# Kernel tuning notes

Hardware: AMD Instinct MI355X
Metric: run time of the kernel (lower is better)

Reference implementation:

```python
import jax, jax.numpy as jnp
import numpy as np
import math

B, S, U, H = 2, 2048, 1024, 16
DK = U // H  # 64


def setup_inputs() -> dict:
    key = jax.random.key(0)
    ks = jax.random.split(key, 12)
    scale = 1.0 / math.sqrt(U)
    inp = {
        "query": jax.random.normal(ks[0], (B, S, U), dtype=jnp.float32),
        "key": jax.random.normal(ks[1], (B, S, U), dtype=jnp.float32),
        "value": jax.random.normal(ks[2], (B, S, U), dtype=jnp.float32),
        # causal mask, broadcast over batch: 1 = attend, 0 = masked
        "mask": jnp.broadcast_to(jnp.tril(jnp.ones((S, S), dtype=bool)), (B, S, S)),
        # nn.Linear params (torch convention: y = x @ W.T + b)
        "Wq": jax.random.uniform(ks[3], (U, U), jnp.float32, -scale, scale),
        "bq": jax.random.uniform(ks[4], (U,), jnp.float32, -scale, scale),
        "Wk": jax.random.uniform(ks[5], (U, U), jnp.float32, -scale, scale),
        "bk": jax.random.uniform(ks[6], (U,), jnp.float32, -scale, scale),
        "Wv": jax.random.uniform(ks[7], (U, U), jnp.float32, -scale, scale),
        "bv": jax.random.uniform(ks[8], (U,), jnp.float32, -scale, scale),
        "Wo": jax.random.uniform(ks[9], (U, U), jnp.float32, -scale, scale),
        "bo": jax.random.uniform(ks[10], (U,), jnp.float32, -scale, scale),
    }
    return inp


def reference(query, key, value, mask, Wq, bq, Wk, bk, Wv, bv, Wo, bo):
    b = query.shape[0]
    # QKV projections -> [b, H, S, DK]
    q = (query @ Wq.T + bq).reshape(b, -1, H, DK).transpose(0, 2, 1, 3)
    k = (key @ Wk.T + bk).reshape(b, -1, H, DK).transpose(0, 2, 1, 3)
    v = (value @ Wv.T + bv).reshape(b, -1, H, DK).transpose(0, 2, 1, 3)
    # scaled dot-product scores [b, H, Sq, Sk]
    scores = jnp.einsum("bhqd,bhkd->bhqk", q, k) / math.sqrt(DK)
    scores = jnp.where(mask[:, None, :, :], scores, jnp.float32(-1e9))
    A = jax.nn.softmax(scores, axis=-1)
    # dropout is eval/identity (p effectively inactive in reference)
    Hout = jnp.einsum("bhqk,bhkd->bhqd", A, v)
    H_concat = Hout.transpose(0, 2, 1, 3).reshape(b, -1, U)
    return H_concat @ Wo.T + bo
```

## Files before the change

### kernel.cpp

```cpp
#include <hip/hip_runtime.h>
#include <math.h>

#define B_NUM 2
#define S_LEN 2048
#define U_DIM 1024
#define H_NUM 16
#define DK 64
#define M_TOT (B_NUM * S_LEN)

typedef __attribute__((ext_vector_type(8))) short bf8;
typedef __attribute__((ext_vector_type(4))) float f4;

__device__ __forceinline__ unsigned short f2bf(float f) {
    union { float f; unsigned int u; } x; x.f = f;
    unsigned int r = x.u + 0x7fffu + ((x.u >> 16) & 1u);
    return (unsigned short)(r >> 16);
}

__device__ __forceinline__ void gl2lds16(const void* g, void* l) {
    __builtin_amdgcn_global_load_lds(
        (const __attribute__((address_space(1))) unsigned int*)g,
        (__attribute__((address_space(3))) unsigned int*)l, 16, 0, 0);
}

struct CvtArgs {
    const float* src[7];
    unsigned short* dst[7];
    int n[7];
};

__global__ __launch_bounds__(256) void convert_bf16(CvtArgs a)
{
    const int seg = blockIdx.y;
    const int i = (blockIdx.x * 256 + threadIdx.x) * 8;
    if (i >= a.n[seg]) return;
    const float* s = a.src[seg] + i;
    float4 v0 = *(const float4*)s;
    float4 v1 = *(const float4*)(s + 4);
    unsigned int p0 = (unsigned)f2bf(v0.x) | ((unsigned)f2bf(v0.y) << 16);
    unsigned int p1 = (unsigned)f2bf(v0.z) | ((unsigned)f2bf(v0.w) << 16);
    unsigned int p2 = (unsigned)f2bf(v1.x) | ((unsigned)f2bf(v1.y) << 16);
    unsigned int p3 = (unsigned)f2bf(v1.z) | ((unsigned)f2bf(v1.w) << 16);
    uint4 o = {p0, p1, p2, p3};
    *(uint4*)(a.dst[seg] + i) = o;
}

struct GemmLds {
    unsigned short As[2][128][32];
    unsigned short Bs[2][128][32];
};

template <int OMODE>
__device__ __forceinline__ void gemm_core(
    GemmLds& S,
    const unsigned short* __restrict__ A, const unsigned short* __restrict__ W,
    const float* __restrict__ bias, void* __restrict__ Cv, float scale,
    int bx, int by)
{
    const int tid = threadIdx.x;
    const int w = tid >> 6, lane = tid & 63;
    const int quad = lane >> 4, cid = lane & 15;
    const int wy = w >> 1, wx = w & 1;
    const int m0 = by * 128, n0 = bx * 128;

    const int row_s = tid >> 1;
    const int sp = tid & 1;
    const int rr = (row_s >> 2) & 3;
    const int p0 = (2 * sp + rr) & 3;
    const int p1 = (2 * sp + 1 + rr) & 3;

    const unsigned short* gA = A + (size_t)(m0 + row_s) * U_DIM + 16 * sp;
    const unsigned short* gB = W + (size_t)(n0 + row_s) * U_DIM + 16 * sp;

    uint4 a0, a1, b0, b1;
#define GPF(k0_) do {                                   \
        a0 = *(const uint4*)(gA + (k0_));               \
        a1 = *(const uint4*)(gA + (k0_) + 8);           \
        b0 = *(const uint4*)(gB + (k0_));               \
        b1 = *(const uint4*)(gB + (k0_) + 8);           \
    } while (0)

    f4 acc[4][4] = {};

    GPF(0);
    *(uint4*)&S.As[0][row_s][p0 * 8] = a0;
    *(uint4*)&S.As[0][row_s][p1 * 8] = a1;
    *(uint4*)&S.Bs[0][row_s][p0 * 8] = b0;
    *(uint4*)&S.Bs[0][row_s][p1 * 8] = b1;
    GPF(32);
    __syncthreads();

#pragma unroll 2
    for (int k0 = 0; k0 < U_DIM; k0 += 32) {
        const int cur = (k0 >> 5) & 1;
        if (k0 + 32 < U_DIM) {
            const int nxt = cur ^ 1;
            *(uint4*)&S.As[nxt][row_s][p0 * 8] = a0;
            *(uint4*)&S.As[nxt][row_s][p1 * 8] = a1;
            *(uint4*)&S.Bs[nxt][row_s][p0 * 8] = b0;
            *(uint4*)&S.Bs[nxt][row_s][p1 * 8] = b1;
            if (k0 + 64 < U_DIM) GPF(k0 + 64);
        }

        bf8 af[4], bfr[4];
#pragma unroll
        for (int mt = 0; mt < 4; ++mt) {
            int row = wy * 64 + mt * 16 + cid;
            int seg = (quad + (row >> 2)) & 3;
            af[mt] = *(const bf8*)&S.As[cur][row][seg * 8];
        }
#pragma unroll
        for (int nt = 0; nt < 4; ++nt) {
            int row = wx * 64 + nt * 16 + cid;
            int seg = (quad + (row >> 2)) & 3;
            bfr[nt] = *(const bf8*)&S.Bs[cur][row][seg * 8];
        }
#pragma unroll
        for (int mt = 0; mt < 4; ++mt)
#pragma unroll
            for (int nt = 0; nt < 4; ++nt)
                acc[mt][nt] = __builtin_amdgcn_mfma_f32_16x16x32_bf16(
                    af[mt], bfr[nt], acc[mt][nt], 0, 0, 0);
        __syncthreads();
    }
#undef GPF

#pragma unroll
    for (int nt = 0; nt < 4; ++nt) {
        int col = n0 + wx * 64 + nt * 16 + cid;
        float bv = bias[col];
#pragma unroll
        for (int mt = 0; mt < 4; ++mt) {
            int rowb = m0 + wy * 64 + mt * 16 + quad * 4;
#pragma unroll
            for (int i = 0; i < 4; ++i) {
                float v = (acc[mt][nt][i] + bv) * scale;
                if constexpr (OMODE == 0) {
                    ((unsigned short*)Cv)[(size_t)(rowb + i) * U_DIM + col] = f2bf(v);
                } else if constexpr (OMODE == 1) {
                    ((float*)Cv)[(size_t)(rowb + i) * U_DIM + col] = v;
                } else {
                    int bb = rowb >> 11;
                    int ss = (rowb & (S_LEN - 1)) + i;
                    size_t idx = ((size_t)(bb * H_NUM + (col >> 6)) * DK + (col & 63))
                                 * S_LEN + ss;
                    ((unsigned short*)Cv)[idx] = f2bf(v);
                }
            }
        }
    }
}

struct QkvArgs {
    const unsigned short* A[3];
    const unsigned short* W[3];
    const float* bias[3];
    unsigned short* C[3];
    float scale[3];
};

__global__ __launch_bounds__(256, 3) void gemm_qkv(QkvArgs a) {
    __shared__ GemmLds S;
    const int L = (int)blockIdx.x + 8 * ((int)blockIdx.y + 32 * (int)blockIdx.z);
    const int xcd = L & 7, j = L >> 3;
    const int z = j >> 5, r = j & 31;
    const int by = xcd * 4 + (r & 3);
    const int bx = r >> 2;
    if (z == 2)
        gemm_core<2>(S, a.A[2], a.W[2], a.bias[2], a.C[2], a.scale[2], bx, by);
    else
        gemm_core<0>(S, a.A[z], a.W[z], a.bias[z], a.C[z], a.scale[z], bx, by);
}

__global__ __launch_bounds__(256, 3) void gemm_obf(
    const unsigned short* __restrict__ A, const unsigned short* __restrict__ W,
    const float* __restrict__ bias, float* __restrict__ C) {
    __shared__ GemmLds S;
    const int L = (int)blockIdx.x + 8 * (int)blockIdx.y;
    const int xcd = L & 7, j = L >> 3;
    const int by = xcd * 4 + (j & 3);
    const int bx = j >> 2;
    gemm_core<1>(S, A, W, bias, C, 1.0f, bx, by);
}

__global__ __launch_bounds__(256, 4) void attn_mfma(
    const unsigned short* __restrict__ Q, const unsigned short* __restrict__ K,
    const unsigned short* __restrict__ VT, unsigned short* __restrict__ O)
{
    __shared__ __align__(16) unsigned short Ks[128][64];
    __shared__ __align__(16) unsigned short Vs[64][128];

    const int L = (int)blockIdx.x + 32 * ((int)blockIdx.y + 16 * (int)blockIdx.z);
    const int xcd = L & 7;
    const int j   = L >> 3;
    const int gl  = j & 3;
    const int i   = j >> 2;
    const int hb  = (xcd << 2) | gl;
    const int h = hb & 15, b = hb >> 4;
    const int px = i & 7, pk = i >> 3;
    const int qt = (pk == 0) ? 31 - px : (pk == 1) ? 16 + px
                 : (pk == 2) ? 15 - px : px;

    const int q0 = qt * 64;
    const int tid = threadIdx.x, w = tid >> 6, lane = tid & 63;
    const int quad = lane >> 4, cid = lane & 15;

#define KFRAG(r, s) (*(const bf8*)&Ks[r][(((s) ^ ((r) & 7)) * 8)])
#define VFRAG(r, s) (*(const bf8*)&Vs[r][(((((s) & 8) | (((s) ^ (r)) & 7))) * 8)])

    unsigned short (*QsA)[64] = (unsigned short (*)[64])&Ks[0][0];
    const int srow8 = lane >> 3;
    const int sw = ((lane & 7) ^ srow8) * 8;
    {
        const unsigned short* qg =
            Q + ((size_t)b * S_LEN + q0 + w * 16 + srow8) * U_DIM + h * DK + sw;
        gl2lds16(qg, &QsA[w * 16][0]);
        gl2lds16(qg + 8 * U_DIM, &QsA[w * 16 + 8][0]);
    }
    __syncthreads();
    const bf8 qfa = *(const bf8*)&QsA[w * 16 + cid][(((quad) ^ (cid & 7)) * 8)];
    const bf8 qfb = *(const bf8*)&QsA[w * 16 + cid][((((quad + 4)) ^ (cid & 7)) * 8)];

    const unsigned short* kgl =
        K + ((size_t)b * S_LEN + w * 32 + srow8) * U_DIM + h * DK + (lane & 7) * 8;
    const int vr0 = lane >> 4;
    const int s16 = lane & 15;
    const unsigned short* vgl =
        VT + ((size_t)(b * H_NUM + h) * DK + w * 16 + vr0) * S_LEN + s16 * 8;
    const int spE = (((s16 & 8) | ((s16 ^ vr0) & 7))) * 8;
    const int spO = (((s16 & 8) | ((s16 ^ (vr0 + 4)) & 7))) * 8;
    const int ksw = ((lane & 7) ^ srow8) * 8;

    uint4 kr0, kr1, kr2, kr3, vq0, vq1, vq2, vq3;
#define PREFETCH(kt_) do {                                                    \
        const unsigned short* kp_ = kgl + (size_t)(kt_) * 128 * U_DIM;        \
        kr0 = *(const uint4*)(kp_);                                           \
        kr1 = *(const uint4*)(kp_ + (size_t)8 * U_DIM);                       \
        kr2 = *(const uint4*)(kp_ + (size_t)16 * U_DIM);                      \
        kr3 = *(const uint4*)(kp_ + (size_t)24 * U_DIM);                      \
        const unsigned short* vp_ = vgl + (kt_) * 128;                        \
        vq0 = *(const uint4*)(vp_);                                           \
        vq1 = *(const uint4*)(vp_ + (size_t)4 * S_LEN);                       \
        vq2 = *(const uint4*)(vp_ + (size_t)8 * S_LEN);                       \
        vq3 = *(const uint4*)(vp_ + (size_t)12 * S_LEN);                      \
    } while (0)

    f4 o[4] = {};
    float l_p = 0.0f;
    const int qrow = q0 + w * 16 + cid;

    const int nkt = (qt >> 1) + 1;
    PREFETCH(0);

    for (int kt = 0; kt < nkt; ++kt) {
        __syncthreads();
        *(uint4*)&Ks[w * 32 + 0  + srow8][ksw] = kr0;
        *(uint4*)&Ks[w * 32 + 8  + srow8][ksw] = kr1;
        *(uint4*)&Ks[w * 32 + 16 + srow8][ksw] = kr2;
        *(uint4*)&Ks[w * 32 + 24 + srow8][ksw] = kr3;
        *(uint4*)&Vs[w * 16 + 0  + vr0][spE] = vq0;
        *(uint4*)&Vs[w * 16 + 4  + vr0][spO] = vq1;
        *(uint4*)&Vs[w * 16 + 8  + vr0][spE] = vq2;
        *(uint4*)&Vs[w * 16 + 12 + vr0][spO] = vq3;
        __syncthreads();
        if (kt + 1 < nkt) PREFETCH(kt + 1);

        f4 sc[8];
#pragma unroll
        for (int t = 0; t < 8; ++t) {
            int r = t * 16 + cid;
            f4 a = {};
            a = __builtin_amdgcn_mfma_f32_16x16x32_bf16(KFRAG(r, quad), qfa, a, 0, 0, 0);
            a = __builtin_amdgcn_mfma_f32_16x16x32_bf16(KFRAG(r, quad + 4), qfb, a, 0, 0, 0);
            sc[t] = a;
        }

        if (kt == nkt - 1) {
#pragma unroll
            for (int t = 0; t < 8; ++t) {
#pragma unroll
                for (int i2 = 0; i2 < 4; ++i2) {
                    int key = kt * 128 + t * 16 + quad * 4 + i2;
                    if (key > qrow) sc[t][i2] = -1e30f;
                }
            }
        }

#pragma unroll
        for (int t = 0; t < 8; ++t) {
#pragma unroll
            for (int i2 = 0; i2 < 4; ++i2) {
                float p = exp2f(sc[t][i2]);
                sc[t][i2] = p;
                l_p += p;
            }
        }

        unsigned int r_[8], r2_[8];
#pragma unroll
        for (int t = 0; t < 8; ++t) {
            asm("v_cvt_pk_bf16_f32 %0, %1, %2"
                : "=v"(r_[t]) : "v"(sc[t][0]), "v"(sc[t][1]));
            asm("v_cvt_pk_bf16_f32 %0, %1, %2"
                : "=v"(r2_[t]) : "v"(sc[t][2]), "v"(sc[t][3]));
        }

        const bool qodd = (quad & 1) != 0;
#pragma unroll
        for (int f = 0; f < 4; ++f) {
            unsigned int xa = r_[2 * f], ya = r_[2 * f + 1];
            asm("v_permlane32_swap_b32 %0, %1" : "+v"(xa), "+v"(ya));
            unsigned int xas = __builtin_amdgcn_ds_swizzle((int)xa, 0x401f);
            unsigned int yas = __builtin_amdgcn_ds_swizzle((int)ya, 0x401f);
            unsigned int xb = r2_[2 * f], yb = r2_[2 * f + 1];
            asm("v_permlane32_swap_b32 %0, %1" : "+v"(xb), "+v"(yb));
            unsigned int xbs = __builtin_amdgcn_ds_swizzle((int)xb, 0x401f);
            unsigned int ybs = __builtin_amdgcn_ds_swizzle((int)yb, 0x401f);
            unsigned int u0 = qodd ? yas : xa;
            unsigned int u1 = qodd ? ybs : xb;
            unsigned int u2 = qodd ? ya : xas;
            unsigned int u3 = qodd ? yb : xbs;
            union { uint4 u; bf8 v; } pf;
            pf.u = (uint4){u0, u1, u2, u3};
#pragma unroll
            for (int t = 0; t < 4; ++t) {
                int r = t * 16 + cid;
                o[t] = __builtin_amdgcn_mfma_f32_16x16x32_bf16(
                    pf.v, VFRAG(r, 4 * f + quad), o[t], 0, 0, 0);
            }
        }
    }
#undef PREFETCH
#undef KFRAG
#undef VFRAG

    float l = l_p;
    l += __shfl_xor(l, 16);
    l += __shfl_xor(l, 32);
    const float inv = 1.0f / l;
#pragma unroll
    for (int i2 = 0; i2 < 4; ++i2) {
        float invi = __shfl(inv, (lane & 48) | (quad * 4 + i2));
        int rowg = q0 + w * 16 + quad * 4 + i2;
        size_t rbase = ((size_t)b * S_LEN + rowg) * U_DIM + h * DK;
#pragma unroll
        for (int t = 0; t < 4; ++t)
            O[rbase + t * 16 + cid] = f2bf(o[t][i2] * invi);
    }
}

extern "C" void kernel_launch(void* const* d_in, const int* in_sizes, int n_in,
                              void* d_out, int out_size, void* d_ws, size_t ws_size,
                              hipStream_t stream)
{
    const float* query = (const float*)d_in[0];
    const float* key   = (const float*)d_in[1];
    const float* value = (const float*)d_in[2];
    const float* Wq = (const float*)d_in[4];
    const float* bq = (const float*)d_in[5];
    const float* Wk = (const float*)d_in[6];
    const float* bk = (const float*)d_in[7];
    const float* Wv = (const float*)d_in[8];
    const float* bv = (const float*)d_in[9];
    const float* Wo = (const float*)d_in[10];
    const float* bo = (const float*)d_in[11];
    float* out = (float*)d_out;

    const size_t ACT = (size_t)M_TOT * U_DIM;
    const size_t WT  = (size_t)U_DIM * U_DIM;

    unsigned short* xq  = (unsigned short*)d_ws;
    unsigned short* xk  = xq + ACT;
    unsigned short* xv  = xk + ACT;
    unsigned short* wqb = xv + ACT;
    unsigned short* wkb = wqb + WT;
    unsigned short* wvb = wkb + WT;
    unsigned short* wob = wvb + WT;
    unsigned short* qg  = wob + WT;
    unsigned short* kg  = qg + ACT;
    unsigned short* vg  = kg + ACT;
    unsigned short* vt  = vg + ACT;
    unsigned short* ao  = vt + ACT;

    CvtArgs ca;
    ca.src[0] = query; ca.dst[0] = xq;  ca.n[0] = (int)ACT;
    ca.src[1] = key;   ca.dst[1] = xk;  ca.n[1] = (int)ACT;
    ca.src[2] = value; ca.dst[2] = xv;  ca.n[2] = (int)ACT;
    ca.src[3] = Wq;    ca.dst[3] = wqb; ca.n[3] = (int)WT;
    ca.src[4] = Wk;    ca.dst[4] = wkb; ca.n[4] = (int)WT;
    ca.src[5] = Wv;    ca.dst[5] = wvb; ca.n[5] = (int)WT;
    ca.src[6] = Wo;    ca.dst[6] = wob; ca.n[6] = (int)WT;
    convert_bf16<<<dim3(ACT / (256 * 8), 7), 256, 0, stream>>>(ca);

    QkvArgs ga;
    ga.A[0] = xq; ga.W[0] = wqb; ga.bias[0] = bq; ga.C[0] = qg;
    ga.scale[0] = 0.125f * 1.44269504088896340736f;
    ga.A[1] = xk; ga.W[1] = wkb; ga.bias[1] = bk; ga.C[1] = kg; ga.scale[1] = 1.0f;
    ga.A[2] = xv; ga.W[2] = wvb; ga.bias[2] = bv; ga.C[2] = vt; ga.scale[2] = 1.0f;
    gemm_qkv<<<dim3(U_DIM / 128, M_TOT / 128, 3), 256, 0, stream>>>(ga);

    attn_mfma<<<dim3(S_LEN / 64, H_NUM, B_NUM), 256, 0, stream>>>(qg, kg, vt, ao);

    gemm_obf<<<dim3(U_DIM / 128, M_TOT / 128), 256, 0, stream>>>(ao, wob, bo, out);
}
```

Baseline: 224.6 us.

## Fuse fp32-to-bf16 conversion into GEMM tile loads, drop separate convert kernel

Removes the standalone conversion kernel that cast activations and weights to bf16 in workspace. The GEMMs now load fp32 tiles directly and pack them to bf16 with v_cvt_pk_bf16_f32 before the LDS store. This avoids one launch and the write-then-reread of bf16 copies. In exchange, each GEMM reads twice the global bytes per tile, repeated across tiles, and uses more registers for the prefetch.

```diff
diff --git a/kernel.cpp b/kernel.cpp
--- a/kernel.cpp
+++ b/kernel.cpp
@@ -17,43 +17,30 @@
     return (unsigned short)(r >> 16);
 }
 
+__device__ __forceinline__ unsigned int pkbf(float a, float b) {
+    unsigned int r;
+    asm("v_cvt_pk_bf16_f32 %0, %1, %2" : "=v"(r) : "v"(a), "v"(b));
+    return r;
+}
+__device__ __forceinline__ uint4 pack8(float4 u, float4 v) {
+    return (uint4){pkbf(u.x, u.y), pkbf(u.z, u.w), pkbf(v.x, v.y), pkbf(v.z, v.w)};
+}
+
 __device__ __forceinline__ void gl2lds16(const void* g, void* l) {
     __builtin_amdgcn_global_load_lds(
         (const __attribute__((address_space(1))) unsigned int*)g,
         (__attribute__((address_space(3))) unsigned int*)l, 16, 0, 0);
 }
 
-struct CvtArgs {
-    const float* src[7];
-    unsigned short* dst[7];
-    int n[7];
-};
-
-__global__ __launch_bounds__(256) void convert_bf16(CvtArgs a)
-{
-    const int seg = blockIdx.y;
-    const int i = (blockIdx.x * 256 + threadIdx.x) * 8;
-    if (i >= a.n[seg]) return;
-    const float* s = a.src[seg] + i;
-    float4 v0 = *(const float4*)s;
-    float4 v1 = *(const float4*)(s + 4);
-    unsigned int p0 = (unsigned)f2bf(v0.x) | ((unsigned)f2bf(v0.y) << 16);
-    unsigned int p1 = (unsigned)f2bf(v0.z) | ((unsigned)f2bf(v0.w) << 16);
-    unsigned int p2 = (unsigned)f2bf(v1.x) | ((unsigned)f2bf(v1.y) << 16);
-    unsigned int p3 = (unsigned)f2bf(v1.z) | ((unsigned)f2bf(v1.w) << 16);
-    uint4 o = {p0, p1, p2, p3};
-    *(uint4*)(a.dst[seg] + i) = o;
-}
-
 struct GemmLds {
     unsigned short As[2][128][32];
     unsigned short Bs[2][128][32];
 };
 
-template <int OMODE>
+template <int OMODE, bool AF32>
 __device__ __forceinline__ void gemm_core(
     GemmLds& S,
-    const unsigned short* __restrict__ A, const unsigned short* __restrict__ W,
+    const void* __restrict__ Av, const float* __restrict__ Wf,
     const float* __restrict__ bias, void* __restrict__ Cv, float scale,
     int bx, int by)
 {
@@ -69,24 +56,46 @@
     const int p0 = (2 * sp + rr) & 3;
     const int p1 = (2 * sp + 1 + rr) & 3;
 
-    const unsigned short* gA = A + (size_t)(m0 + row_s) * U_DIM + 16 * sp;
-    const unsigned short* gB = W + (size_t)(n0 + row_s) * U_DIM + 16 * sp;
-
-    uint4 a0, a1, b0, b1;
-#define GPF(k0_) do {                                   \
-        a0 = *(const uint4*)(gA + (k0_));               \
-        a1 = *(const uint4*)(gA + (k0_) + 8);           \
-        b0 = *(const uint4*)(gB + (k0_));               \
-        b1 = *(const uint4*)(gB + (k0_) + 8);           \
+    const unsigned short* gA =
+        (const unsigned short*)Av + (size_t)(m0 + row_s) * U_DIM + 16 * sp;
+    const float* gAf =
+        (const float*)Av + (size_t)(m0 + row_s) * U_DIM + 16 * sp;
+    const float* gBf = Wf + (size_t)(n0 + row_s) * U_DIM + 16 * sp;
+
+    uint4 a0, a1;
+    float4 fa0, fa1, fa2, fa3, fb0, fb1, fb2, fb3;
+#define GPF(k0_) do {                                       \
+        if constexpr (AF32) {                               \
+            fa0 = *(const float4*)(gAf + (k0_));            \
+            fa1 = *(const float4*)(gAf + (k0_) + 4);        \
+            fa2 = *(const float4*)(gAf + (k0_) + 8);        \
+            fa3 = *(const float4*)(gAf + (k0_) + 12);       \
+        } else {                                            \
+            a0 = *(const uint4*)(gA + (k0_));               \
+            a1 = *(const uint4*)(gA + (k0_) + 8);           \
+        }                                                   \
+        fb0 = *(const float4*)(gBf + (k0_));                \
+        fb1 = *(const float4*)(gBf + (k0_) + 4);            \
+        fb2 = *(const float4*)(gBf + (k0_) + 8);            \
+        fb3 = *(const float4*)(gBf + (k0_) + 12);           \
     } while (0)
 
+#define STORE(buf_) do {                                    \
+        uint4 ta0, ta1;                                     \
+        if constexpr (AF32) {                               \
+            ta0 = pack8(fa0, fa1); ta1 = pack8(fa2, fa3);   \
+        } else { ta0 = a0; ta1 = a1; }                      \
+        uint4 tb0 = pack8(fb0, fb1), tb1 = pack8(fb2, fb3); \
+        *(uint4*)&S.As[buf_][row_s][p0 * 8] = ta0;          \
+        *(uint4*)&S.As[buf_][row_s][p1 * 8] = ta1;          \
+        *(uint4*)&S.Bs[buf_][row_s][p0 * 8] = tb0;          \
+        *(uint4*)&S.Bs[buf_][row_s][p1 * 8] = tb1;          \
+    } while (0)
+
     f4 acc[4][4] = {};
 
     GPF(0);
-    *(uint4*)&S.As[0][row_s][p0 * 8] = a0;
-    *(uint4*)&S.As[0][row_s][p1 * 8] = a1;
-    *(uint4*)&S.Bs[0][row_s][p0 * 8] = b0;
-    *(uint4*)&S.Bs[0][row_s][p1 * 8] = b1;
+    STORE(0);
     GPF(32);
     __syncthreads();
 
@@ -94,11 +103,7 @@
     for (int k0 = 0; k0 < U_DIM; k0 += 32) {
         const int cur = (k0 >> 5) & 1;
         if (k0 + 32 < U_DIM) {
-            const int nxt = cur ^ 1;
-            *(uint4*)&S.As[nxt][row_s][p0 * 8] = a0;
-            *(uint4*)&S.As[nxt][row_s][p1 * 8] = a1;
-            *(uint4*)&S.Bs[nxt][row_s][p0 * 8] = b0;
-            *(uint4*)&S.Bs[nxt][row_s][p1 * 8] = b1;
+            STORE(cur ^ 1);
             if (k0 + 64 < U_DIM) GPF(k0 + 64);
         }
 
@@ -124,6 +129,7 @@
         __syncthreads();
     }
 #undef GPF
+#undef STORE
 
 #pragma unroll
     for (int nt = 0; nt < 4; ++nt) {
@@ -152,8 +158,8 @@
 }
 
 struct QkvArgs {
-    const unsigned short* A[3];
-    const unsigned short* W[3];
+    const void* A[3];
+    const float* W[3];
     const float* bias[3];
     unsigned short* C[3];
     float scale[3];
@@ -167,20 +173,20 @@
     const int by = xcd * 4 + (r & 3);
     const int bx = r >> 2;
     if (z == 2)
-        gemm_core<2>(S, a.A[2], a.W[2], a.bias[2], a.C[2], a.scale[2], bx, by);
+        gemm_core<2, true>(S, a.A[2], a.W[2], a.bias[2], a.C[2], a.scale[2], bx, by);
     else
-        gemm_core<0>(S, a.A[z], a.W[z], a.bias[z], a.C[z], a.scale[z], bx, by);
+        gemm_core<0, true>(S, a.A[z], a.W[z], a.bias[z], a.C[z], a.scale[z], bx, by);
 }
 
 __global__ __launch_bounds__(256, 3) void gemm_obf(
-    const unsigned short* __restrict__ A, const unsigned short* __restrict__ W,
+    const unsigned short* __restrict__ A, const float* __restrict__ W,
     const float* __restrict__ bias, float* __restrict__ C) {
     __shared__ GemmLds S;
     const int L = (int)blockIdx.x + 8 * (int)blockIdx.y;
     const int xcd = L & 7, j = L >> 3;
     const int by = xcd * 4 + (j & 3);
     const int bx = j >> 2;
-    gemm_core<1>(S, A, W, bias, C, 1.0f, bx, by);
+    gemm_core<1, false>(S, A, W, bias, C, 1.0f, bx, by);
 }
 
 __global__ __launch_bounds__(256, 4) void attn_mfma(
@@ -299,10 +305,8 @@
         unsigned int r_[8], r2_[8];
 #pragma unroll
         for (int t = 0; t < 8; ++t) {
-            asm("v_cvt_pk_bf16_f32 %0, %1, %2"
-                : "=v"(r_[t]) : "v"(sc[t][0]), "v"(sc[t][1]));
-            asm("v_cvt_pk_bf16_f32 %0, %1, %2"
-                : "=v"(r2_[t]) : "v"(sc[t][2]), "v"(sc[t][3]));
+            r_[t]  = pkbf(sc[t][0], sc[t][1]);
+            r2_[t] = pkbf(sc[t][2], sc[t][3]);
         }
 
         const bool qodd = (quad & 1) != 0;
@@ -367,39 +371,20 @@
     float* out = (float*)d_out;
 
     const size_t ACT = (size_t)M_TOT * U_DIM;
-    const size_t WT  = (size_t)U_DIM * U_DIM;
-
-    unsigned short* xq  = (unsigned short*)d_ws;
-    unsigned short* xk  = xq + ACT;
-    unsigned short* xv  = xk + ACT;
-    unsigned short* wqb = xv + ACT;
-    unsigned short* wkb = wqb + WT;
-    unsigned short* wvb = wkb + WT;
-    unsigned short* wob = wvb + WT;
-    unsigned short* qg  = wob + WT;
-    unsigned short* kg  = qg + ACT;
-    unsigned short* vg  = kg + ACT;
-    unsigned short* vt  = vg + ACT;
-    unsigned short* ao  = vt + ACT;
-
-    CvtArgs ca;
-    ca.src[0] = query; ca.dst[0] = xq;  ca.n[0] = (int)ACT;
-    ca.src[1] = key;   ca.dst[1] = xk;  ca.n[1] = (int)ACT;
-    ca.src[2] = value; ca.dst[2] = xv;  ca.n[2] = (int)ACT;
-    ca.src[3] = Wq;    ca.dst[3] = wqb; ca.n[3] = (int)WT;
-    ca.src[4] = Wk;    ca.dst[4] = wkb; ca.n[4] = (int)WT;
-    ca.src[5] = Wv;    ca.dst[5] = wvb; ca.n[5] = (int)WT;
-    ca.src[6] = Wo;    ca.dst[6] = wob; ca.n[6] = (int)WT;
-    convert_bf16<<<dim3(ACT / (256 * 8), 7), 256, 0, stream>>>(ca);
+
+    unsigned short* qg = (unsigned short*)d_ws;
+    unsigned short* kg = qg + ACT;
+    unsigned short* vt = kg + ACT;
+    unsigned short* ao = vt + ACT;
 
     QkvArgs ga;
-    ga.A[0] = xq; ga.W[0] = wqb; ga.bias[0] = bq; ga.C[0] = qg;
+    ga.A[0] = query; ga.W[0] = Wq; ga.bias[0] = bq; ga.C[0] = qg;
     ga.scale[0] = 0.125f * 1.44269504088896340736f;
-    ga.A[1] = xk; ga.W[1] = wkb; ga.bias[1] = bk; ga.C[1] = kg; ga.scale[1] = 1.0f;
-    ga.A[2] = xv; ga.W[2] = wvb; ga.bias[2] = bv; ga.C[2] = vt; ga.scale[2] = 1.0f;
+    ga.A[1] = key;   ga.W[1] = Wk; ga.bias[1] = bk; ga.C[1] = kg; ga.scale[1] = 1.0f;
+    ga.A[2] = value; ga.W[2] = Wv; ga.bias[2] = bv; ga.C[2] = vt; ga.scale[2] = 1.0f;
     gemm_qkv<<<dim3(U_DIM / 128, M_TOT / 128, 3), 256, 0, stream>>>(ga);
 
     attn_mfma<<<dim3(S_LEN / 64, H_NUM, B_NUM), 256, 0, stream>>>(qg, kg, vt, ao);
 
-    gemm_obf<<<dim3(U_DIM / 128, M_TOT / 128), 256, 0, stream>>>(ao, wob, bo, out);
-}
+    gemm_obf<<<dim3(U_DIM / 128, M_TOT / 128), 256, 0, stream>>>(ao, Wo, bo, out);
+}
```

Result: slower. 248.4 us (+10.6%).

## Stage GEMM tiles with direct global-to-LDS loads and use packed bf16 conversion

Applied to the files above, without the earlier changes.

The GEMM main loop now fills shared memory with global_load_lds, loading straight into LDS with a swizzled source column, instead of loading into registers and then storing to LDS. The sync moves to the top of the loop. This frees registers and removes the VGPR-to-LDS store instructions. The fp32-to-bf16 convert kernel now uses the hardware v_cvt_pk_bf16_f32 instruction in place of manual rounding, and an unused workspace buffer is dropped. The prefetch distance shrinks to one stage, so less global latency is hidden per iteration.

```diff
diff --git a/kernel.cpp b/kernel.cpp
--- a/kernel.cpp
+++ b/kernel.cpp
@@ -15,6 +15,12 @@
     union { float f; unsigned int u; } x; x.f = f;
     unsigned int r = x.u + 0x7fffu + ((x.u >> 16) & 1u);
     return (unsigned short)(r >> 16);
+}
+
+__device__ __forceinline__ unsigned int pkbf(float a, float b) {
+    unsigned int r;
+    asm("v_cvt_pk_bf16_f32 %0, %1, %2" : "=v"(r) : "v"(a), "v"(b));
+    return r;
 }
 
 __device__ __forceinline__ void gl2lds16(const void* g, void* l) {
@@ -37,11 +43,8 @@
     const float* s = a.src[seg] + i;
     float4 v0 = *(const float4*)s;
     float4 v1 = *(const float4*)(s + 4);
-    unsigned int p0 = (unsigned)f2bf(v0.x) | ((unsigned)f2bf(v0.y) << 16);
-    unsigned int p1 = (unsigned)f2bf(v0.z) | ((unsigned)f2bf(v0.w) << 16);
-    unsigned int p2 = (unsigned)f2bf(v1.x) | ((unsigned)f2bf(v1.y) << 16);
-    unsigned int p3 = (unsigned)f2bf(v1.z) | ((unsigned)f2bf(v1.w) << 16);
-    uint4 o = {p0, p1, p2, p3};
+    uint4 o = {pkbf(v0.x, v0.y), pkbf(v0.z, v0.w),
+               pkbf(v1.x, v1.y), pkbf(v1.z, v1.w)};
     *(uint4*)(a.dst[seg] + i) = o;
 }
 
@@ -63,44 +66,29 @@
     const int wy = w >> 1, wx = w & 1;
     const int m0 = by * 128, n0 = bx * 128;
 
-    const int row_s = tid >> 1;
-    const int sp = tid & 1;
-    const int rr = (row_s >> 2) & 3;
-    const int p0 = (2 * sp + rr) & 3;
-    const int p1 = (2 * sp + 1 + rr) & 3;
-
-    const unsigned short* gA = A + (size_t)(m0 + row_s) * U_DIM + 16 * sp;
-    const unsigned short* gB = W + (size_t)(n0 + row_s) * U_DIM + 16 * sp;
-
-    uint4 a0, a1, b0, b1;
-#define GPF(k0_) do {                                   \
-        a0 = *(const uint4*)(gA + (k0_));               \
-        a1 = *(const uint4*)(gA + (k0_) + 8);           \
-        b0 = *(const uint4*)(gB + (k0_));               \
-        b1 = *(const uint4*)(gB + (k0_) + 8);           \
+    const int l2 = lane >> 2, s4 = lane & 3;
+    const int ra = 32 * w + l2;
+    const int rr = (ra >> 2) & 3;
+    const int cseg = (((s4 + 4) - rr) & 3) * 8;
+    const unsigned short* gAs = A + (size_t)(m0 + ra) * U_DIM + cseg;
+    const unsigned short* gBs = W + (size_t)(n0 + ra) * U_DIM + cseg;
+
+#define STAGE(buf_, k_) do {                                               \
+        gl2lds16(gAs + (k_),              &S.As[buf_][32 * w][0]);         \
+        gl2lds16(gAs + (k_) + 16 * U_DIM, &S.As[buf_][32 * w + 16][0]);    \
+        gl2lds16(gBs + (k_),              &S.Bs[buf_][32 * w][0]);         \
+        gl2lds16(gBs + (k_) + 16 * U_DIM, &S.Bs[buf_][32 * w + 16][0]);    \
     } while (0)
 
     f4 acc[4][4] = {};
 
-    GPF(0);
-    *(uint4*)&S.As[0][row_s][p0 * 8] = a0;
-    *(uint4*)&S.As[0][row_s][p1 * 8] = a1;
-    *(uint4*)&S.Bs[0][row_s][p0 * 8] = b0;
-    *(uint4*)&S.Bs[0][row_s][p1 * 8] = b1;
-    GPF(32);
-    __syncthreads();
+    STAGE(0, 0);
 
 #pragma unroll 2
     for (int k0 = 0; k0 < U_DIM; k0 += 32) {
         const int cur = (k0 >> 5) & 1;
-        if (k0 + 32 < U_DIM) {
-            const int nxt = cur ^ 1;
-            *(uint4*)&S.As[nxt][row_s][p0 * 8] = a0;
-            *(uint4*)&S.As[nxt][row_s][p1 * 8] = a1;
-            *(uint4*)&S.Bs[nxt][row_s][p0 * 8] = b0;
-            *(uint4*)&S.Bs[nxt][row_s][p1 * 8] = b1;
-            if (k0 + 64 < U_DIM) GPF(k0 + 64);
-        }
+        __syncthreads();
+        if (k0 + 32 < U_DIM) STAGE(cur ^ 1, k0 + 32);
 
         bf8 af[4], bfr[4];
 #pragma unroll
@@ -121,9 +109,8 @@
             for (int nt = 0; nt < 4; ++nt)
                 acc[mt][nt] = __builtin_amdgcn_mfma_f32_16x16x32_bf16(
                     af[mt], bfr[nt], acc[mt][nt], 0, 0, 0);
-        __syncthreads();
-    }
-#undef GPF
+    }
+#undef STAGE
 
 #pragma unroll
     for (int nt = 0; nt < 4; ++nt) {
@@ -299,10 +286,8 @@
         unsigned int r_[8], r2_[8];
 #pragma unroll
         for (int t = 0; t < 8; ++t) {
-            asm("v_cvt_pk_bf16_f32 %0, %1, %2"
-                : "=v"(r_[t]) : "v"(sc[t][0]), "v"(sc[t][1]));
-            asm("v_cvt_pk_bf16_f32 %0, %1, %2"
-                : "=v"(r2_[t]) : "v"(sc[t][2]), "v"(sc[t][3]));
+            r_[t]  = pkbf(sc[t][0], sc[t][1]);
+            r2_[t] = pkbf(sc[t][2], sc[t][3]);
         }
 
         const bool qodd = (quad & 1) != 0;
@@ -378,8 +363,7 @@
     unsigned short* wob = wvb + WT;
     unsigned short* qg  = wob + WT;
     unsigned short* kg  = qg + ACT;
-    unsigned short* vg  = kg + ACT;
-    unsigned short* vt  = vg + ACT;
+    unsigned short* vt  = kg + ACT;
     unsigned short* ao  = vt + ACT;
 
     CvtArgs ca;
```

Measured after the change: 224.9 us. Within noise of the previous version (+0.2%).
